# Performance work log

Hardware: AMD Instinct MI355X
Metric: run time of the kernel (lower is better)

The kernel has to match this reference:

```python
import jax, jax.numpy as jnp
import numpy as np


def setup_inputs() -> dict:
    key = jax.random.key(0)
    k1, k2 = jax.random.split(key)
    x = jax.random.normal(k1, (3000, 800, 8), dtype=jnp.float32)
    y = jax.random.normal(k2, (3000, 800, 8), dtype=jnp.float32)
    return {"x": x, "y": y}


def _cumtrapz(a):
    # torch.cumulative_trapezoid along last axis (unit spacing): len nt-1
    return jnp.cumsum(0.5 * (a[:, 1:] + a[:, :-1]), axis=1)


def _wd1d(x, y):
    nt = x.shape[0]
    # flatten (ntraces, nchannels) -> batch of independent 1D traces [N, nt]
    syn = x.reshape(nt, -1).T
    obs = y.reshape(nt, -1).T
    # per trace-pair joint minimum (torch.min(torch.min(syn), torch.min(obs)))
    mind = jnp.minimum(syn.min(axis=1, keepdims=True), obs.min(axis=1, keepdims=True))
    syn = syn - mind
    obs = obs - mind
    cdf_syn = _cumtrapz(syn)                                  # [N, nt-1]
    cdf_obs = _cumtrapz(obs)                                  # [N, nt-1]
    syn_norm = cdf_syn / jnp.sum(cdf_syn, axis=1, keepdims=True)
    obs_norm = cdf_obs / jnp.sum(cdf_obs, axis=1, keepdims=True)
    # torch.searchsorted default (right=False) == jnp side='left'
    idx = jax.vmap(lambda a, v: jnp.searchsorted(a, v, side='left'))(obs_norm, syn_norm)
    idx = jnp.minimum(idx, nt - 1)                            # clamp; t[idx] == idx since t = arange(nt)
    t_tail = jnp.arange(1, nt, dtype=jnp.int32)               # t[1:]
    diff = (t_tail[None, :] - idx).astype(syn_norm.dtype)
    return jnp.sum(diff * diff * syn_norm)


def reference(x, y):
    return _wd1d(x, y)
```

## Files before the change

kernel.cpp:

```cpp
#include <hip/hip_runtime.h>

#define NT   3000
#define NK   2999
#define NTR  6400
#define CCH  32
#define KCH  94
#define BLK  256

#define TRIW 4498500.0f

__global__ __launch_bounds__(BLK) void kA(
    const float* __restrict__ X, const float* __restrict__ Y,
    float* __restrict__ ssx, float* __restrict__ ssy,
    float* __restrict__ wsx, float* __restrict__ wsy,
    float* __restrict__ cmn)
{
    const int n = blockIdx.x * BLK + threadIdx.x;
    const int c = blockIdx.y;
    const int j0 = c * KCH;
    const int j1 = min(NK, j0 + KCH);

    float xp = X[j0 * NTR + n];
    float yp = Y[j0 * NTR + n];
    float mn = fminf(xp, yp);
    float sxs = 0.f, sys = 0.f, wxs = 0.f, wys = 0.f;

    for (int j = j0; j < j1; ++j) {
        const float xn = X[(j + 1) * NTR + n];
        const float yn = Y[(j + 1) * NTR + n];
        const float sx = 0.5f * (xp + xn);
        const float sy = 0.5f * (yp + yn);
        const float wgt = (float)(NK - j);
        sxs += sx; sys += sy;
        wxs = fmaf(sx, wgt, wxs);
        wys = fmaf(sy, wgt, wys);
        mn = fminf(mn, fminf(xn, yn));
        xp = xn; yp = yn;
    }

    const int o = c * NTR + n;
    ssx[o] = sxs; ssy[o] = sys;
    wsx[o] = wxs; wsy[o] = wys;
    cmn[o] = mn;
}

__global__ __launch_bounds__(BLK) void kB(
    const float* __restrict__ ssx, const float* __restrict__ ssy,
    const float* __restrict__ wsx, const float* __restrict__ wsy,
    const float* __restrict__ cmn,
    float* __restrict__ offx, float* __restrict__ offy,
    float* __restrict__ mindA, float* __restrict__ SsynA,
    float* __restrict__ SobsA, float* __restrict__ out)
{
    const int n = blockIdx.x * BLK + threadIdx.x;
    if (blockIdx.x == 0 && threadIdx.x == 0) out[0] = 0.0f;

    float mn = 3.4e38f;
    for (int c = 0; c < CCH; ++c) mn = fminf(mn, cmn[c * NTR + n]);

    float rx = 0.f, ry = 0.f, wx = 0.f, wy = 0.f;
    for (int c = 0; c < CCH; ++c) {
        const int o = c * NTR + n;
        offx[o] = rx; offy[o] = ry;
        rx += ssx[o]; ry += ssy[o];
        wx += wsx[o]; wy += wsy[o];
    }

    mindA[n] = mn;
    SsynA[n] = wx - mn * TRIW;
    SobsA[n] = wy - mn * TRIW;
}

__global__ __launch_bounds__(BLK) void kC(
    const float* __restrict__ X, const float* __restrict__ Y,
    const float* __restrict__ offx, const float* __restrict__ offy,
    const float* __restrict__ mindA, const float* __restrict__ SsynA,
    const float* __restrict__ SobsA, float* __restrict__ out)
{
    const int n = blockIdx.x * BLK + threadIdx.x;
    const int c = blockIdx.y;
    const int j0 = c * KCH;
    const int j1 = min(NK, j0 + KCH);

    const float mind = mindA[n];
    const float Ssyn = SsynA[n];
    const float Sobs = SobsA[n];
    const float invS = 1.0f / Ssyn;

    float cs = offx[c * NTR + n];
    float xp = X[j0 * NTR + n];

    int   m  = -1;
    float co = 0.f;
    float yp = 0.f;
    float acc = 0.f;

    for (int k = j0; k < j1; ++k) {
        const float xn = X[(k + 1) * NTR + n];
        cs += 0.5f * (xp + xn);
        xp = xn;
        const float syn_p  = cs - (float)(k + 1) * mind;
        const float target = syn_p * Sobs;

        if (m < 0) {
            int cc = 0;
            for (int c2 = CCH - 1; c2 >= 1; --c2) {
                const float v = (offy[c2 * NTR + n] - (float)(c2 * KCH) * mind) * Ssyn;
                if (v < target) { cc = c2; break; }
            }
            m  = cc * KCH;
            co = offy[cc * NTR + n];
            yp = Y[m * NTR + n];
        }

        while (m < NK) {
            const float yn = Y[(m + 1) * NTR + n];
            const float s  = 0.5f * (yp + yn);
            const float obs_p = co + s - (float)(m + 1) * mind;
            if (obs_p * Ssyn < target) { co += s; yp = yn; ++m; }
            else break;
        }

        const float diff = (float)(k + 1 - m);
        acc = fmaf(diff * diff, syn_p * invS, acc);
    }

    __shared__ float red[BLK];
    red[threadIdx.x] = acc;
    __syncthreads();
    for (int s = BLK / 2; s > 0; s >>= 1) {
        if (threadIdx.x < s) red[threadIdx.x] += red[threadIdx.x + s];
        __syncthreads();
    }
    if (threadIdx.x == 0) atomicAdd(out, red[0]);
}

extern "C" void kernel_launch(void* const* d_in, const int* in_sizes, int n_in,
                              void* d_out, int out_size, void* d_ws, size_t ws_size,
                              hipStream_t stream)
{
    const float* X = (const float*)d_in[0];
    const float* Y = (const float*)d_in[1];
    float* out = (float*)d_out;

    float* w = (float*)d_ws;
    float* ssx  = w;
    float* ssy  = ssx  + CCH * NTR;
    float* wsx  = ssy  + CCH * NTR;
    float* wsy  = wsx  + CCH * NTR;
    float* cmn  = wsy  + CCH * NTR;
    float* offx = cmn  + CCH * NTR;
    float* offy = offx + CCH * NTR;
    float* mindA = offy + CCH * NTR;
    float* SsynA = mindA + NTR;
    float* SobsA = SsynA + NTR;

    dim3 grid2(NTR / BLK, CCH);
    dim3 grid1(NTR / BLK);
    dim3 blk(BLK);

    kA<<<grid2, blk, 0, stream>>>(X, Y, ssx, ssy, wsx, wsy, cmn);
    kB<<<grid1, blk, 0, stream>>>(ssx, ssy, wsx, wsy, cmn,
                                  offx, offy, mindA, SsynA, SobsA, out);
    kC<<<grid2, blk, 0, stream>>>(X, Y, offx, offy, mindA, SsynA, SobsA, out);
}
```

Measured before the change: 384.8 us.

## Transpose Y into trace-major trapezoid rows and precompute per-chunk search starts

The first pass now tiles 64x64 through shared memory. It writes a transposed, trace-major array of Y trapezoid increments, so the merge walk in the final kernel reads each trace contiguously instead of striding across traces. Per-trace weighted sums and minima are combined with atomics, and the middle kernel precomputes each chunk's starting search chunk as a byte, replacing the per-thread backward scan. Chunks shrink to 64 samples, and the single-atomic output becomes per-block partials plus a final reduction kernel. The cost is writing and reading an extra ~77MB transposed buffer, plus two memsets.

```diff
diff --git a/kernel.cpp b/kernel.cpp
--- a/kernel.cpp
+++ b/kernel.cpp
@@ -3,136 +3,207 @@
 #define NT   3000
 #define NK   2999
 #define NTR  6400
-#define CCH  32
-#define KCH  94
-#define BLK  256
-
 #define TRIW 4498500.0f
-
-__global__ __launch_bounds__(BLK) void kA(
+#define FINF 3.4e38f
+
+#define TSTR 3008
+#define CB   47
+#define GT   64
+#define NPART 1175
+
+__device__ __forceinline__ unsigned fmap(float f) {
+    unsigned u = __float_as_uint(f);
+    return (u & 0x80000000u) ? ~u : (u | 0x80000000u);
+}
+__device__ __forceinline__ float funmap(unsigned u) {
+    u = (u & 0x80000000u) ? (u & 0x7FFFFFFFu) : ~u;
+    return __uint_as_float(u);
+}
+
+__global__ __launch_bounds__(256) void kT(
     const float* __restrict__ X, const float* __restrict__ Y,
+    float* __restrict__ sTy,
     float* __restrict__ ssx, float* __restrict__ ssy,
-    float* __restrict__ wsx, float* __restrict__ wsy,
-    float* __restrict__ cmn)
-{
-    const int n = blockIdx.x * BLK + threadIdx.x;
+    float* __restrict__ wsxA, float* __restrict__ wsyA,
+    unsigned* __restrict__ mnUx, unsigned* __restrict__ mnUy)
+{
+    __shared__ float t[65][65];
+    __shared__ float pS[4][GT], pW[4][GT], pM[4][GT];
+    const int lane = threadIdx.x & 63;
+    const int wv   = threadIdx.x >> 6;
+    const int n0 = blockIdx.x * 64;
+    const int j0 = blockIdx.y * 64;
+    const int z  = blockIdx.z;
+    const float* __restrict__ src = z ? Y : X;
+    float* __restrict__ ssA = z ? ssy : ssx;
+    float* __restrict__ wA  = z ? wsyA : wsxA;
+    unsigned* __restrict__ mU = z ? mnUy : mnUx;
+
+    #pragma unroll
+    for (int i = 0; i < 17; ++i) {
+        const int r = wv + 4 * i;
+        if (r < 65) {
+            const int jr = j0 + r;
+            if (jr < NT) t[r][lane] = src[(size_t)jr * NTR + n0 + lane];
+        }
+    }
+    __syncthreads();
+
+    if (z) {
+        const int j = j0 + lane;
+        const bool vs = (j < NK);
+        for (int rr = 0; rr < 16; ++rr) {
+            const int row = wv * 16 + rr;
+            const float a0 = t[lane][row];
+            const float a1 = t[lane + 1][row];
+            sTy[(size_t)(n0 + row) * TSTR + j0 + lane] = vs ? 0.5f * (a0 + a1) : 0.f;
+        }
+    }
+
+    {
+        const int r0 = wv * 16;
+        float sum = 0.f, wsum = 0.f, mn = FINF;
+        float aprev = t[r0][lane];
+        #pragma unroll 4
+        for (int rr = 0; rr < 16; ++rr) {
+            const int jr = j0 + r0 + rr;
+            const float anext = t[r0 + rr + 1][lane];
+            if (jr < NT) mn = fminf(mn, aprev);
+            if (jr < NK) {
+                const float s = 0.5f * (aprev + anext);
+                sum += s;
+                wsum = fmaf(s, (float)(NK - jr), wsum);
+            }
+            aprev = anext;
+        }
+        pS[wv][lane] = sum; pW[wv][lane] = wsum; pM[wv][lane] = mn;
+    }
+    __syncthreads();
+    if (threadIdx.x < GT) {
+        const int l = threadIdx.x;
+        const float S = pS[0][l] + pS[1][l] + pS[2][l] + pS[3][l];
+        const float W = pW[0][l] + pW[1][l] + pW[2][l] + pW[3][l];
+        const float M = fminf(fminf(pM[0][l], pM[1][l]), fminf(pM[2][l], pM[3][l]));
+        ssA[blockIdx.y * NTR + n0 + l] = S;
+        atomicAdd(&wA[n0 + l], W);
+        atomicMin(&mU[n0 + l], fmap(M));
+    }
+}
+
+__global__ __launch_bounds__(256) void kB2(
+    float* __restrict__ ssx, float* __restrict__ ssy,
+    const float* __restrict__ wsxA, const float* __restrict__ wsyA,
+    const unsigned* __restrict__ mnUx, const unsigned* __restrict__ mnUy,
+    float* __restrict__ mindA, float* __restrict__ SsA, float* __restrict__ SoA,
+    unsigned char* __restrict__ qstA)
+{
+    __shared__ float tA[CB][GT + 1];
+    __shared__ float tB[CB][GT + 1];
+    const int n0 = blockIdx.x * GT;
+    const int tid = threadIdx.x, lane = tid & 63, crow = tid >> 6;
+
+    for (int c = crow; c < CB; c += 4) {
+        tA[c][lane] = ssx[c * NTR + n0 + lane];
+        tB[c][lane] = ssy[c * NTR + n0 + lane];
+    }
+    __syncthreads();
+
+    if (tid < GT) {
+        const float mn = fminf(funmap(mnUx[n0 + tid]), funmap(mnUy[n0 + tid]));
+        const float Ss = wsxA[n0 + tid] - mn * TRIW;
+        const float So = wsyA[n0 + tid] - mn * TRIW;
+        mindA[n0 + tid] = mn; SsA[n0 + tid] = Ss; SoA[n0 + tid] = So;
+
+        float rx = 0.f, ry = 0.f;
+        for (int c = 0; c < CB; ++c) {
+            const float tx = tA[c][tid], ty = tB[c][tid];
+            tA[c][tid] = rx; tB[c][tid] = ry;
+            rx += tx; ry += ty;
+        }
+        int q = 0;
+        qstA[n0 + tid] = 0;
+        for (int c = 1; c < CB; ++c) {
+            const float tgt = (tA[c][tid] - (float)(c * 64) * mn) * So;
+            while (q + 1 < CB) {
+                const float ov = (tB[q + 1][tid] - (float)((q + 1) * 64) * mn) * Ss;
+                if (ov < tgt) ++q; else break;
+            }
+            qstA[c * NTR + n0 + tid] = (unsigned char)q;
+        }
+    }
+    __syncthreads();
+    for (int c = crow; c < CB; c += 4) {
+        ssx[c * NTR + n0 + lane] = tA[c][lane];
+        ssy[c * NTR + n0 + lane] = tB[c][lane];
+    }
+}
+
+__global__ __launch_bounds__(256) void kC3(
+    const float* __restrict__ X, const float* __restrict__ sTy,
+    const float* __restrict__ ssxS, const float* __restrict__ ssyS,
+    const float* __restrict__ mindA, const float* __restrict__ SsA,
+    const float* __restrict__ SoA, const unsigned char* __restrict__ qstA,
+    float* __restrict__ partial)
+{
+    const int n = blockIdx.x * 256 + threadIdx.x;
     const int c = blockIdx.y;
-    const int j0 = c * KCH;
-    const int j1 = min(NK, j0 + KCH);
-
-    float xp = X[j0 * NTR + n];
-    float yp = Y[j0 * NTR + n];
-    float mn = fminf(xp, yp);
-    float sxs = 0.f, sys = 0.f, wxs = 0.f, wys = 0.f;
-
-    for (int j = j0; j < j1; ++j) {
-        const float xn = X[(j + 1) * NTR + n];
-        const float yn = Y[(j + 1) * NTR + n];
-        const float sx = 0.5f * (xp + xn);
-        const float sy = 0.5f * (yp + yn);
-        const float wgt = (float)(NK - j);
-        sxs += sx; sys += sy;
-        wxs = fmaf(sx, wgt, wxs);
-        wys = fmaf(sy, wgt, wys);
-        mn = fminf(mn, fminf(xn, yn));
-        xp = xn; yp = yn;
-    }
-
-    const int o = c * NTR + n;
-    ssx[o] = sxs; ssy[o] = sys;
-    wsx[o] = wxs; wsy[o] = wys;
-    cmn[o] = mn;
-}
-
-__global__ __launch_bounds__(BLK) void kB(
-    const float* __restrict__ ssx, const float* __restrict__ ssy,
-    const float* __restrict__ wsx, const float* __restrict__ wsy,
-    const float* __restrict__ cmn,
-    float* __restrict__ offx, float* __restrict__ offy,
-    float* __restrict__ mindA, float* __restrict__ SsynA,
-    float* __restrict__ SobsA, float* __restrict__ out)
-{
-    const int n = blockIdx.x * BLK + threadIdx.x;
-    if (blockIdx.x == 0 && threadIdx.x == 0) out[0] = 0.0f;
-
-    float mn = 3.4e38f;
-    for (int c = 0; c < CCH; ++c) mn = fminf(mn, cmn[c * NTR + n]);
-
-    float rx = 0.f, ry = 0.f, wx = 0.f, wy = 0.f;
-    for (int c = 0; c < CCH; ++c) {
-        const int o = c * NTR + n;
-        offx[o] = rx; offy[o] = ry;
-        rx += ssx[o]; ry += ssy[o];
-        wx += wsx[o]; wy += wsy[o];
-    }
-
-    mindA[n] = mn;
-    SsynA[n] = wx - mn * TRIW;
-    SobsA[n] = wy - mn * TRIW;
-}
-
-__global__ __launch_bounds__(BLK) void kC(
-    const float* __restrict__ X, const float* __restrict__ Y,
-    const float* __restrict__ offx, const float* __restrict__ offy,
-    const float* __restrict__ mindA, const float* __restrict__ SsynA,
-    const float* __restrict__ SobsA, float* __restrict__ out)
-{
-    const int n = blockIdx.x * BLK + threadIdx.x;
-    const int c = blockIdx.y;
-    const int j0 = c * KCH;
-    const int j1 = min(NK, j0 + KCH);
+    const int j0 = c * 64;
+    const int j1 = min(NK, j0 + 64);
 
     const float mind = mindA[n];
-    const float Ssyn = SsynA[n];
-    const float Sobs = SobsA[n];
-    const float invS = 1.0f / Ssyn;
-
-    float cs = offx[c * NTR + n];
-    float xp = X[j0 * NTR + n];
-
-    int   m  = -1;
-    float co = 0.f;
-    float yp = 0.f;
+    const float Ss = SsA[n];
+    const float So = SoA[n];
+
+    float cs = ssxS[c * NTR + n];
+    float xp = X[(size_t)j0 * NTR + n];
+
+    const float* __restrict__ syr = sTy + (size_t)n * TSTR;
+    int m;
+    float cy;
+    {
+        const int q = (int)qstA[c * NTR + n];
+        m = q * 64;
+        cy = ssyS[q * NTR + n] + syr[m];
+    }
+
     float acc = 0.f;
-
     for (int k = j0; k < j1; ++k) {
-        const float xn = X[(k + 1) * NTR + n];
-        cs += 0.5f * (xp + xn);
-        xp = xn;
-        const float syn_p  = cs - (float)(k + 1) * mind;
-        const float target = syn_p * Sobs;
-
-        if (m < 0) {
-            int cc = 0;
-            for (int c2 = CCH - 1; c2 >= 1; --c2) {
-                const float v = (offy[c2 * NTR + n] - (float)(c2 * KCH) * mind) * Ssyn;
-                if (v < target) { cc = c2; break; }
-            }
-            m  = cc * KCH;
-            co = offy[cc * NTR + n];
-            yp = Y[m * NTR + n];
-        }
-
-        while (m < NK) {
-            const float yn = Y[(m + 1) * NTR + n];
-            const float s  = 0.5f * (yp + yn);
-            const float obs_p = co + s - (float)(m + 1) * mind;
-            if (obs_p * Ssyn < target) { co += s; yp = yn; ++m; }
-            else break;
-        }
-
+        const float xn = X[(size_t)(k + 1) * NTR + n];
+        cs += 0.5f * (xp + xn); xp = xn;
+        const float synp = cs - (float)(k + 1) * mind;
+        const float target = synp * So;
+        while (m < NK && (cy - (float)(m + 1) * mind) * Ss < target) {
+            ++m;
+            cy += syr[m];
+        }
         const float diff = (float)(k + 1 - m);
-        acc = fmaf(diff * diff, syn_p * invS, acc);
-    }
-
-    __shared__ float red[BLK];
+        acc = fmaf(diff * diff, synp, acc);
+    }
+    acc /= Ss;
+
+    __shared__ float red[256];
     red[threadIdx.x] = acc;
     __syncthreads();
-    for (int s = BLK / 2; s > 0; s >>= 1) {
+    for (int s = 128; s > 0; s >>= 1) {
         if (threadIdx.x < s) red[threadIdx.x] += red[threadIdx.x + s];
         __syncthreads();
     }
-    if (threadIdx.x == 0) atomicAdd(out, red[0]);
+    if (threadIdx.x == 0) partial[blockIdx.y * 25 + blockIdx.x] = red[0];
+}
+
+__global__ __launch_bounds__(256) void kD(
+    const float* __restrict__ partial, float* __restrict__ out)
+{
+    float v = 0.f;
+    for (int i = threadIdx.x; i < NPART; i += 256) v += partial[i];
+    __shared__ float red[256];
+    red[threadIdx.x] = v;
+    __syncthreads();
+    for (int s = 128; s > 0; s >>= 1) {
+        if (threadIdx.x < s) red[threadIdx.x] += red[threadIdx.x + s];
+        __syncthreads();
+    }
+    if (threadIdx.x == 0) out[0] = red[0];
 }
 
 extern "C" void kernel_launch(void* const* d_in, const int* in_sizes, int n_in,
@@ -144,23 +215,26 @@
     float* out = (float*)d_out;
 
     float* w = (float*)d_ws;
-    float* ssx  = w;
-    float* ssy  = ssx  + CCH * NTR;
-    float* wsx  = ssy  + CCH * NTR;
-    float* wsy  = wsx  + CCH * NTR;
-    float* cmn  = wsy  + CCH * NTR;
-    float* offx = cmn  + CCH * NTR;
-    float* offy = offx + CCH * NTR;
-    float* mindA = offy + CCH * NTR;
-    float* SsynA = mindA + NTR;
-    float* SobsA = SsynA + NTR;
-
-    dim3 grid2(NTR / BLK, CCH);
-    dim3 grid1(NTR / BLK);
-    dim3 blk(BLK);
-
-    kA<<<grid2, blk, 0, stream>>>(X, Y, ssx, ssy, wsx, wsy, cmn);
-    kB<<<grid1, blk, 0, stream>>>(ssx, ssy, wsx, wsy, cmn,
-                                  offx, offy, mindA, SsynA, SobsA, out);
-    kC<<<grid2, blk, 0, stream>>>(X, Y, offx, offy, mindA, SsynA, SobsA, out);
-}
+    float* sTy  = w;
+    float* ssx  = sTy + (size_t)NTR * TSTR;
+    float* ssy  = ssx + CB * NTR;
+    float* wsxA = ssy + CB * NTR;
+    float* wsyA = wsxA + NTR;
+    unsigned* mnU = (unsigned*)(wsyA + NTR);
+    float* mindA = (float*)(mnU + 2 * NTR);
+    float* SsA   = mindA + NTR;
+    float* SoA   = SsA + NTR;
+    float* partial = SoA + NTR;
+    unsigned char* qstA = (unsigned char*)(partial + 2048);
+
+    hipMemsetAsync(wsxA, 0, 2 * NTR * sizeof(float), stream);
+    hipMemsetAsync(mnU, 0xFF, 2 * NTR * sizeof(unsigned), stream);
+
+    kT<<<dim3(100, 47, 2), 256, 0, stream>>>(X, Y, sTy, ssx, ssy,
+                                             wsxA, wsyA, mnU, mnU + NTR);
+    kB2<<<100, 256, 0, stream>>>(ssx, ssy, wsxA, wsyA, mnU, mnU + NTR,
+                                 mindA, SsA, SoA, qstA);
+    kC3<<<dim3(25, 47), 256, 0, stream>>>(X, sTy, ssx, ssy,
+                                          mindA, SsA, SoA, qstA, partial);
+    kD<<<1, 256, 0, stream>>>(partial, out);
+}
```

Measured after the change: 438.0 us. +13.8%, slower.
